# Performance work log

Measured on AMD Instinct MI355X. Metric: run time of the kernel, lower is better.

Reference implementation:

```python
import jax, jax.numpy as jnp
import numpy as np


def _orthogonal_matrix(vectors):
    # Q = I @ H1 @ H2 @ ... ; each H = I - 2 v v^T applied as a rank-1 update:
    # Q @ H = Q - 2 (Q v) v^T  (same math as explicit matmul, O(d^2) per reflection)
    dim = vectors.shape[1]
    eye = jnp.eye(dim, dtype=vectors.dtype)

    def step(Q, v):
        vn = v / (jnp.linalg.norm(v) + 1e-8)
        Q = Q - 2.0 * jnp.outer(Q @ vn, vn)
        return Q, None

    Q, _ = jax.lax.scan(step, eye, vectors)
    return Q


def setup_inputs() -> dict:
    key = jax.random.key(0)
    k1, k2 = jax.random.split(key)
    dim, n_reflections, batch = 2048, 30, 16384
    x = jax.random.normal(k1, (batch, dim), dtype=jnp.float32)
    vectors = jax.random.normal(k2, (n_reflections, dim), dtype=jnp.float32)
    bias = jnp.zeros((dim,), dtype=jnp.float32)
    return {"x": x, "vectors": vectors, "bias": bias}


def reference(x, vectors, bias):
    Q = _orthogonal_matrix(vectors)      # [dim, dim]
    return x @ Q + bias                  # [batch, dim]
```

## Files before the change

kernel.cpp:

```cpp
#include <hip/hip_runtime.h>
#include <math.h>

#define DIM   2048
#define NREF  30
#define KPAD  32
#define BATCH 16384

typedef __attribute__((ext_vector_type(8))) short short8;
typedef __attribute__((ext_vector_type(4))) float f32x4;

#define WS_VN   0
#define WS_G    61440
#define WS_T    62464
#define WS_FP1  63488
#define WS_FP2  96256

__device__ __forceinline__ unsigned short f2bf(float f) {
    unsigned u = __float_as_uint(f);
    u += 0x7FFF + ((u >> 16) & 1);
    return (unsigned short)(u >> 16);
}

__global__ void k_prep(const float* __restrict__ vec, float* __restrict__ vn,
                       float* __restrict__ G) {
    int b = blockIdx.x, t = threadIdx.x;
    __shared__ float wsum[3][4];
    if (b < NREF) {
        const float* v = vec + b * DIM;
        float s = 0.f;
        for (int d = t; d < DIM; d += 256) { float xv = v[d]; s += xv * xv; }
        #pragma unroll
        for (int off = 32; off > 0; off >>= 1) s += __shfl_down(s, off);
        if ((t & 63) == 0) wsum[0][t >> 6] = s;
        __syncthreads();
        float tot = wsum[0][0] + wsum[0][1] + wsum[0][2] + wsum[0][3];
        float scale = 1.f / (sqrtf(tot) + 1e-8f);
        float* o = vn + b * DIM;
        for (int d = t; d < DIM; d += 256) o[d] = v[d] * scale;
    } else {
        int idx = b - NREF;
        int i = idx / NREF, j = idx % NREF;
        const float* a = vec + i * DIM;
        const float* c = vec + j * DIM;
        float sab = 0.f, saa = 0.f, sbb = 0.f;
        for (int d = t; d < DIM; d += 256) {
            float av = a[d], cv = c[d];
            sab += av * cv; saa += av * av; sbb += cv * cv;
        }
        #pragma unroll
        for (int off = 32; off > 0; off >>= 1) {
            sab += __shfl_down(sab, off);
            saa += __shfl_down(saa, off);
            sbb += __shfl_down(sbb, off);
        }
        if ((t & 63) == 0) { wsum[0][t >> 6] = sab; wsum[1][t >> 6] = saa; wsum[2][t >> 6] = sbb; }
        __syncthreads();
        if (t == 0) {
            float tab = wsum[0][0] + wsum[0][1] + wsum[0][2] + wsum[0][3];
            float taa = wsum[1][0] + wsum[1][1] + wsum[1][2] + wsum[1][3];
            float tbb = wsum[2][0] + wsum[2][1] + wsum[2][2] + wsum[2][3];
            G[i * NREF + j] = tab / ((sqrtf(taa) + 1e-8f) * (sqrtf(tbb) + 1e-8f));
        }
    }
}

__global__ void k_T2(const float* __restrict__ G, float* __restrict__ T) {
    int t = threadIdx.x;
    __shared__ float Gs[NREF * NREF];
    __shared__ float Ts[NREF][NREF];
    for (int idx = t; idx < NREF * NREF; idx += 64) {
        Gs[idx] = G[idx];
        Ts[idx / NREF][idx % NREF] = 0.f;
    }
    __syncthreads();
    if (t < NREF) {
        Ts[t][t] = 2.f;
        for (int j = t + 1; j < NREF; j++) {
            float val = 0.f;
            for (int mm = t; mm < j; mm++) val += Ts[t][mm] * Gs[mm * NREF + j];
            Ts[t][j] = -2.f * val;
        }
    }
    __syncthreads();
    for (int idx = t; idx < NREF * NREF; idx += 64) T[idx] = Ts[idx / NREF][idx % NREF];
}

__global__ void k_mid(const float* __restrict__ vn, const float* __restrict__ T,
                      unsigned short* __restrict__ fp1, unsigned short* __restrict__ fp2) {
    int b = blockIdx.x, t = threadIdx.x;
    if (b < 8) {
        __shared__ float W2s[256][33];
        int d = b * 256 + t;
        float vr[NREF];
        #pragma unroll
        for (int j = 0; j < NREF; j++) vr[j] = vn[j * DIM + d];
        #pragma unroll
        for (int k = 0; k < KPAD; k++) {
            float acc = 0.f;
            if (k < NREF)
                for (int j = 0; j <= k; j++) acc += vr[j] * T[j * NREF + k];
            W2s[t][k] = acc;
        }
        __syncthreads();
        short8* out = (short8*)fp1;
        #pragma unroll
        for (int u = 0; u < 4; u++) {
            int lf = t * 4 + u;
            int ks_l = lf >> 7, nt = (lf >> 6) & 1, lane = lf & 63;
            int q = lane >> 4, n = lane & 15;
            short8 v;
            #pragma unroll
            for (int j = 0; j < 8; j++)
                v[j] = (short)f2bf(W2s[ks_l * 32 + q * 8 + j][nt * 16 + n]);
            out[((b * 8 + ks_l) * 2 + nt) * 64 + lane] = v;
        }
    } else {
        int g = (b - 8) * 256 + t;
        int ct = g >> 6, lane = g & 63;
        int q = lane >> 4, n = lane & 15;
        short8 v;
        #pragma unroll
        for (int j = 0; j < 8; j++) {
            int k = q * 8 + j;
            float f = (k < NREF) ? vn[(size_t)k * DIM + ct * 16 + n] : 0.f;
            v[j] = (short)f2bf(f);
        }
        ((short8*)fp2)[ct * 64 + lane] = v;
    }
}

__global__ __launch_bounds__(256, 2) void k_fused(const float* __restrict__ x,
                                                  const short8* __restrict__ fp1,
                                                  const short8* __restrict__ fp2,
                                                  const float* __restrict__ bias,
                                                  float* __restrict__ y) {
    int tid = threadIdx.x;
    int wave = tid >> 6, lane = tid & 63;
    int m = lane & 15, q = lane >> 4;
    int r0 = blockIdx.x * 16;
    int kb = wave * 512;

    const float* xp = x + (size_t)(r0 + m) * DIM + kb + q * 8;

    f32x4 xr[32];
    #pragma unroll
    for (int ks = 0; ks < 16; ks++) {
        xr[2 * ks]     = *(const f32x4*)(xp + ks * 32);
        xr[2 * ks + 1] = *(const f32x4*)(xp + ks * 32 + 4);
    }

    f32x4 acc0 = {0.f, 0.f, 0.f, 0.f};
    f32x4 acc1 = {0.f, 0.f, 0.f, 0.f};
    #pragma unroll
    for (int ks = 0; ks < 16; ks++) {
        f32x4 xa = xr[2 * ks], xb = xr[2 * ks + 1];
        short8 a;
        a[0] = (short)f2bf(xa[0]); a[1] = (short)f2bf(xa[1]);
        a[2] = (short)f2bf(xa[2]); a[3] = (short)f2bf(xa[3]);
        a[4] = (short)f2bf(xb[0]); a[5] = (short)f2bf(xb[1]);
        a[6] = (short)f2bf(xb[2]); a[7] = (short)f2bf(xb[3]);
        int ksg = wave * 16 + ks;
        short8 b0 = fp1[(ksg * 2 + 0) * 64 + lane];
        short8 b1 = fp1[(ksg * 2 + 1) * 64 + lane];
        acc0 = __builtin_amdgcn_mfma_f32_16x16x32_bf16(a, b0, acc0, 0, 0, 0);
        acc1 = __builtin_amdgcn_mfma_f32_16x16x32_bf16(a, b1, acc1, 0, 0, 0);
    }

    __shared__ f32x4 red[4][64][2];
    __shared__ unsigned short Slds[16][32];
    red[wave][lane][0] = acc0;
    red[wave][lane][1] = acc1;
    __syncthreads();
    if (tid < 64) {
        f32x4 s0 = red[0][tid][0], s1 = red[0][tid][1];
        #pragma unroll
        for (int w = 1; w < 4; w++) { s0 += red[w][tid][0]; s1 += red[w][tid][1]; }
        int mq = tid & 15, qq = tid >> 4;
        #pragma unroll
        for (int reg = 0; reg < 4; reg++) {
            Slds[qq * 4 + reg][mq]      = f2bf(s0[reg]);
            Slds[qq * 4 + reg][16 + mq] = f2bf(s1[reg]);
        }
    }
    __syncthreads();

    short8 aS = *(const short8*)&Slds[m][q * 8];
    f32x4 zero = {0.f, 0.f, 0.f, 0.f};
    __shared__ float Pb[4][2][16][36];
    const float* bp = bias + kb + q * 8;
    float* yp0 = y + (size_t)(r0 + m) * DIM + kb + q * 8;

    #pragma unroll
    for (int u = 0; u < 16; u++) {
        int pb = u & 1;
        short8 b0 = fp2[(wave * 32 + 2 * u) * 64 + lane];
        short8 b1 = fp2[(wave * 32 + 2 * u + 1) * 64 + lane];
        f32x4 p0 = __builtin_amdgcn_mfma_f32_16x16x32_bf16(aS, b0, zero, 0, 0, 0);
        f32x4 p1 = __builtin_amdgcn_mfma_f32_16x16x32_bf16(aS, b1, zero, 0, 0, 0);
        #pragma unroll
        for (int reg = 0; reg < 4; reg++) {
            Pb[wave][pb][q * 4 + reg][m]      = p0[reg];
            Pb[wave][pb][q * 4 + reg][16 + m] = p1[reg];
        }
        asm volatile("s_waitcnt lgkmcnt(0)" ::: "memory");
        f32x4 pr0 = *(const f32x4*)&Pb[wave][pb][m][q * 8];
        f32x4 pr1 = *(const f32x4*)&Pb[wave][pb][m][q * 8 + 4];
        f32x4 bb0 = *(const f32x4*)(bp + u * 32);
        f32x4 bb1 = *(const f32x4*)(bp + u * 32 + 4);
        f32x4 o0 = xr[2 * u] + bb0 - pr0;
        f32x4 o1 = xr[2 * u + 1] + bb1 - pr1;
        *(f32x4*)(yp0 + u * 32)     = o0;
        *(f32x4*)(yp0 + u * 32 + 4) = o1;
    }
}

extern "C" void kernel_launch(void* const* d_in, const int* in_sizes, int n_in,
                              void* d_out, int out_size, void* d_ws, size_t ws_size,
                              hipStream_t stream) {
    const float* x    = (const float*)d_in[0];
    const float* vec  = (const float*)d_in[1];
    const float* bias = (const float*)d_in[2];
    float* out = (float*)d_out;
    float* ws  = (float*)d_ws;

    float* vn = ws + WS_VN;
    float* G  = ws + WS_G;
    float* T  = ws + WS_T;
    unsigned short* fp1 = (unsigned short*)(ws + WS_FP1);
    unsigned short* fp2 = (unsigned short*)(ws + WS_FP2);

    k_prep<<<NREF + NREF * NREF, 256, 0, stream>>>(vec, vn, G);
    k_T2<<<1, 64, 0, stream>>>(G, T);
    k_mid<<<40, 256, 0, stream>>>(vn, T, fp1, fp2);
    k_fused<<<BATCH / 16, 256, 0, stream>>>(x, (const short8*)fp1, (const short8*)fp2, bias, out);
}
```

Measured before the change: 277.5 us.

## Drop register-cached x rows, reload x in epilogue, raise occupancy

The fused kernel no longer keeps its 16x512 slice of x in 128 registers per lane. x is re-read from global memory in the second stage, and the MFMA output is consumed directly in its native lane layout, with scalar loads and stores per element instead of an LDS transpose. Launch bounds go from 2 to 4 blocks per SM and unrolling is reduced so the kernel fits. This trades register pressure and the LDS round-trip for a second read of x, which may hit in cache, and for scalar, less coalesced 4-byte global accesses.

```diff
diff --git a/kernel.cpp b/kernel.cpp
--- a/kernel.cpp
+++ b/kernel.cpp
@@ -129,7 +129,7 @@
     }
 }
 
-__global__ __launch_bounds__(256, 2) void k_fused(const float* __restrict__ x,
+__global__ __launch_bounds__(256, 4) void k_fused(const float* __restrict__ x,
                                                   const short8* __restrict__ fp1,
                                                   const short8* __restrict__ fp2,
                                                   const float* __restrict__ bias,
@@ -142,18 +142,12 @@
 
     const float* xp = x + (size_t)(r0 + m) * DIM + kb + q * 8;
 
-    f32x4 xr[32];
-    #pragma unroll
-    for (int ks = 0; ks < 16; ks++) {
-        xr[2 * ks]     = *(const f32x4*)(xp + ks * 32);
-        xr[2 * ks + 1] = *(const f32x4*)(xp + ks * 32 + 4);
-    }
-
     f32x4 acc0 = {0.f, 0.f, 0.f, 0.f};
     f32x4 acc1 = {0.f, 0.f, 0.f, 0.f};
-    #pragma unroll
+    #pragma unroll 4
     for (int ks = 0; ks < 16; ks++) {
-        f32x4 xa = xr[2 * ks], xb = xr[2 * ks + 1];
+        f32x4 xa = *(const f32x4*)(xp + ks * 32);
+        f32x4 xb = *(const f32x4*)(xp + ks * 32 + 4);
         short8 a;
         a[0] = (short)f2bf(xa[0]); a[1] = (short)f2bf(xa[1]);
         a[2] = (short)f2bf(xa[2]); a[3] = (short)f2bf(xa[3]);
@@ -186,31 +180,28 @@
 
     short8 aS = *(const short8*)&Slds[m][q * 8];
     f32x4 zero = {0.f, 0.f, 0.f, 0.f};
-    __shared__ float Pb[4][2][16][36];
-    const float* bp = bias + kb + q * 8;
-    float* yp0 = y + (size_t)(r0 + m) * DIM + kb + q * 8;
-
-    #pragma unroll
-    for (int u = 0; u < 16; u++) {
-        int pb = u & 1;
-        short8 b0 = fp2[(wave * 32 + 2 * u) * 64 + lane];
-        short8 b1 = fp2[(wave * 32 + 2 * u + 1) * 64 + lane];
+    int c0 = wave * 512;
+    int rbase = r0 + q * 4;
+
+    #pragma unroll 4
+    for (int t = 0; t < 32; t += 2) {
+        short8 b0 = fp2[(wave * 32 + t) * 64 + lane];
+        short8 b1 = fp2[(wave * 32 + t + 1) * 64 + lane];
         f32x4 p0 = __builtin_amdgcn_mfma_f32_16x16x32_bf16(aS, b0, zero, 0, 0, 0);
         f32x4 p1 = __builtin_amdgcn_mfma_f32_16x16x32_bf16(aS, b1, zero, 0, 0, 0);
+        int cc0 = c0 + t * 16 + m;
+        int cc1 = cc0 + 16;
+        float bi0 = bias[cc0];
+        float bi1 = bias[cc1];
+        const float* xc0 = x + (size_t)rbase * DIM + cc0;
+        const float* xc1 = x + (size_t)rbase * DIM + cc1;
+        float* yc0 = y + (size_t)rbase * DIM + cc0;
+        float* yc1 = y + (size_t)rbase * DIM + cc1;
         #pragma unroll
         for (int reg = 0; reg < 4; reg++) {
-            Pb[wave][pb][q * 4 + reg][m]      = p0[reg];
-            Pb[wave][pb][q * 4 + reg][16 + m] = p1[reg];
-        }
-        asm volatile("s_waitcnt lgkmcnt(0)" ::: "memory");
-        f32x4 pr0 = *(const f32x4*)&Pb[wave][pb][m][q * 8];
-        f32x4 pr1 = *(const f32x4*)&Pb[wave][pb][m][q * 8 + 4];
-        f32x4 bb0 = *(const f32x4*)(bp + u * 32);
-        f32x4 bb1 = *(const f32x4*)(bp + u * 32 + 4);
-        f32x4 o0 = xr[2 * u] + bb0 - pr0;
-        f32x4 o1 = xr[2 * u + 1] + bb1 - pr1;
-        *(f32x4*)(yp0 + u * 32)     = o0;
-        *(f32x4*)(yp0 + u * 32 + 4) = o1;
+            yc0[(size_t)reg * DIM] = xc0[(size_t)reg * DIM] + bi0 - p0[reg];
+            yc1[(size_t)reg * DIM] = xc1[(size_t)reg * DIM] + bi1 - p1[reg];
+        }
     }
 }
 
```

New measurement: 277.9 us. No clear change (+0.1%).
